# Kernel tuning notes

Measured on AMD Instinct MI355X. Metric: run time of the kernel, lower is better.

Reference implementation:

```python
import jax, jax.numpy as jnp
import numpy as np

EPS = 1e-10


def _cotangent(V, F):
    # V: (B,N,3) float, F: (B,Fc,3) int -> C: (B,Fc,3) cotangent weights for edges 23,31,12
    gather = jax.vmap(lambda v, f: v[f])  # (N,3),(Fc,3) -> (Fc,3,3)
    vi = gather(V, F)
    v1, v2, v3 = vi[:, :, 0, :], vi[:, :, 1, :], vi[:, :, 2, :]
    l1 = jnp.sqrt(((v2 - v3) ** 2).sum(-1))
    l2 = jnp.sqrt(((v3 - v1) ** 2).sum(-1))
    l3 = jnp.sqrt(((v1 - v2) ** 2).sum(-1))
    sp = (l1 + l2 + l3) * 0.5
    inside = sp * (sp - l1) * (sp - l2) * (sp - l3)
    inside = jnp.maximum(inside, 0.0)
    A = 2.0 * jnp.sqrt(inside)
    cot23 = l2 ** 2 + l3 ** 2 - l1 ** 2
    cot31 = l1 ** 2 + l3 ** 2 - l2 ** 2
    cot12 = l1 ** 2 + l2 ** 2 - l3 ** 2
    C = jnp.stack([cot23, cot31, cot12], axis=2) / (A[:, :, None] + EPS) / 4.0
    C = jnp.where(A[:, :, None] == 0.0, 0.0, C)
    return C


def setup_inputs() -> dict:
    key = jax.random.key(0)
    k1, k2 = jax.random.split(key)
    B, N, Fc = 8, 100000, 200000
    V = jax.random.normal(k1, (B, N, 3), dtype=jnp.float32)
    F = jax.random.randint(k2, (B, Fc, 3), 0, N, dtype=jnp.int64)
    return {"V": V, "F": F}


def reference(V, F):
    B, N, _ = V.shape
    BN = B * N
    # Laplacian weights are built once from V and treated as constants
    # (the original torch autograd.Function never differentiates through L).
    C = _cotangent(jax.lax.stop_gradient(V), F)  # (B,Fc,3)
    offset = (jnp.arange(B, dtype=F.dtype) * N)[:, None, None]
    Fb = (F + offset).reshape(-1, 3)             # (B*Fc,3) global vertex ids
    rows = Fb[:, jnp.array([1, 2, 0])].reshape(-1)
    cols = Fb[:, jnp.array([2, 0, 1])].reshape(-1)
    w = C.reshape(-1)                             # matches rows/cols ordering

    Vf = V.reshape(BN, 3)
    # Lx where L = A + A^T - diag(rowsum(A + A^T)), A = sparse(rows,cols,w)
    out = jnp.zeros((BN, 3), dtype=V.dtype)
    out = out.at[rows].add(w[:, None] * Vf[cols])
    out = out.at[cols].add(w[:, None] * Vf[rows])
    deg = jnp.zeros((BN,), dtype=V.dtype)
    deg = deg.at[rows].add(w).at[cols].add(w)
    out = out - deg[:, None] * Vf
    return out.reshape(B, N, 3)
```

## Files before the change

### kernel.cpp

```cpp
#include <hip/hip_runtime.h>

#define NBATCH 8
#define NSEG   4

#define RANGE_BIG  13312
#define RANGE_SM   5120

struct I3 { int a, b, c; };
struct P3 { float x, y, z; };

__device__ __forceinline__ void cot_weights(
    const P3& p0, const P3& p1, const P3& p2,
    float& w0, float& w1, float& w2)
{
    const float EPSf = 1e-10f;
    float dx, dy, dz;
    dx = p1.x - p2.x; dy = p1.y - p2.y; dz = p1.z - p2.z;
    float l1 = sqrtf(dx * dx + dy * dy + dz * dz);
    dx = p2.x - p0.x; dy = p2.y - p0.y; dz = p2.z - p0.z;
    float l2 = sqrtf(dx * dx + dy * dy + dz * dz);
    dx = p0.x - p1.x; dy = p0.y - p1.y; dz = p0.z - p1.z;
    float l3 = sqrtf(dx * dx + dy * dy + dz * dz);

    float sp = (l1 + l2 + l3) * 0.5f;
    float inside = sp * (sp - l1) * (sp - l2) * (sp - l3);
    inside = fmaxf(inside, 0.0f);
    float A = 2.0f * sqrtf(inside);
    float denom = A + EPSf;

    float l1s = l1 * l1, l2s = l2 * l2, l3s = l3 * l3;
    w0 = (l2s + l3s - l1s) / denom * 0.25f;
    w1 = (l1s + l3s - l2s) / denom * 0.25f;
    w2 = (l1s + l2s - l3s) / denom * 0.25f;
    if (A == 0.0f) { w0 = 0.0f; w1 = 0.0f; w2 = 0.0f; }
}

__device__ __forceinline__ void gather_body(
    const float* __restrict__ V, const int* __restrict__ F,
    float* __restrict__ part, float* lacc,
    int N, int Fc, int BN3, int range, int nr, int nthreads)
{
    int b  = blockIdx.x % NBATCH;
    int t  = blockIdx.x / NBATCH;
    int r  = t / NSEG;
    int s  = t % NSEG;
    if (r >= nr) return;

    int lo = r * range;
    int hi = min(lo + range, N);
    unsigned rlen = (unsigned)(hi - lo);
    int len3 = (hi - lo) * 3;

    for (int i = threadIdx.x; i < len3; i += nthreads) lacc[i] = 0.0f;
    __syncthreads();

    int fps = (Fc + NSEG - 1) / NSEG;
    int f0 = s * fps;
    int f1 = min(f0 + fps, Fc);

    const int*   Fb = F + (size_t)b * Fc * 3;
    const float* Vb = V + (size_t)b * N * 3;

    for (int f = f0 + (int)threadIdx.x; f < f1; f += nthreads) {
        I3 idx = *reinterpret_cast<const I3*>(Fb + (size_t)f * 3);
        unsigned u0 = (unsigned)(idx.a - lo);
        unsigned u1 = (unsigned)(idx.b - lo);
        unsigned u2 = (unsigned)(idx.c - lo);
        bool in0 = u0 < rlen, in1 = u1 < rlen, in2 = u2 < rlen;
        if (!(in0 || in1 || in2)) continue;

        P3 p0 = *reinterpret_cast<const P3*>(Vb + (size_t)idx.a * 3);
        P3 p1 = *reinterpret_cast<const P3*>(Vb + (size_t)idx.b * 3);
        P3 p2 = *reinterpret_cast<const P3*>(Vb + (size_t)idx.c * 3);

        float w0, w1, w2;
        cot_weights(p0, p1, p2, w0, w1, w2);

        if (in0) {
            atomicAdd(&lacc[u0 * 3 + 0], w1 * (p2.x - p0.x) + w2 * (p1.x - p0.x));
            atomicAdd(&lacc[u0 * 3 + 1], w1 * (p2.y - p0.y) + w2 * (p1.y - p0.y));
            atomicAdd(&lacc[u0 * 3 + 2], w1 * (p2.z - p0.z) + w2 * (p1.z - p0.z));
        }
        if (in1) {
            atomicAdd(&lacc[u1 * 3 + 0], w0 * (p2.x - p1.x) + w2 * (p0.x - p1.x));
            atomicAdd(&lacc[u1 * 3 + 1], w0 * (p2.y - p1.y) + w2 * (p0.y - p1.y));
            atomicAdd(&lacc[u1 * 3 + 2], w0 * (p2.z - p1.z) + w2 * (p0.z - p1.z));
        }
        if (in2) {
            atomicAdd(&lacc[u2 * 3 + 0], w0 * (p1.x - p2.x) + w1 * (p0.x - p2.x));
            atomicAdd(&lacc[u2 * 3 + 1], w0 * (p1.y - p2.y) + w1 * (p0.y - p2.y));
            atomicAdd(&lacc[u2 * 3 + 2], w0 * (p1.z - p2.z) + w1 * (p0.z - p2.z));
        }
    }
    __syncthreads();

    float* dst = part + (size_t)s * BN3 + ((size_t)b * N + lo) * 3;
    for (int i = threadIdx.x; i < len3; i += nthreads) dst[i] = lacc[i];
}

__global__ void __launch_bounds__(1024, 1) cot_gather_big(
    const float* __restrict__ V, const int* __restrict__ F,
    float* __restrict__ part, int N, int Fc, int BN3)
{
    extern __shared__ float lacc_dyn[];
    int nr = (N + RANGE_BIG - 1) / RANGE_BIG;
    gather_body(V, F, part, lacc_dyn, N, Fc, BN3, RANGE_BIG, nr, 1024);
}

__global__ void __launch_bounds__(512) cot_gather_sm(
    const float* __restrict__ V, const int* __restrict__ F,
    float* __restrict__ part, int N, int Fc, int BN3)
{
    __shared__ float lacc_st[RANGE_SM * 3];
    int nr = (N + RANGE_SM - 1) / RANGE_SM;
    gather_body(V, F, part, lacc_st, N, Fc, BN3, RANGE_SM, nr, 512);
}

__global__ void __launch_bounds__(256) cot_merge4(
    const float* __restrict__ part, float* __restrict__ out, int BN3)
{
    int i = blockIdx.x * blockDim.x + threadIdx.x;
    int n4 = BN3 >> 2;
    if (i >= n4) return;
    float4 a = ((const float4*)part)[i];
#pragma unroll
    for (int s = 1; s < NSEG; ++s) {
        float4 p = ((const float4*)(part + (size_t)s * BN3))[i];
        a.x += p.x; a.y += p.y; a.z += p.z; a.w += p.w;
    }
    ((float4*)out)[i] = a;
}

__global__ void __launch_bounds__(256) cot_merge1(
    const float* __restrict__ part, float* __restrict__ out, int BN3)
{
    int i = blockIdx.x * blockDim.x + threadIdx.x;
    if (i >= BN3) return;
    float v = part[i];
#pragma unroll
    for (int s = 1; s < NSEG; ++s) v += part[(size_t)s * BN3 + i];
    out[i] = v;
}

__global__ void __launch_bounds__(256) cot_face_add9(
    const float* __restrict__ V, const int* __restrict__ F,
    float* __restrict__ out, int N, int Fc)
{
    int idx = blockIdx.x * blockDim.x + threadIdx.x;
    int total = NBATCH * Fc;
    if (idx >= total) return;

    int b = idx / Fc;
    I3 ix = *reinterpret_cast<const I3*>(F + (size_t)idx * 3);
    int vb = b * N;
    int g0 = vb + ix.a, g1 = vb + ix.b, g2 = vb + ix.c;

    P3 p0 = *reinterpret_cast<const P3*>(V + (size_t)g0 * 3);
    P3 p1 = *reinterpret_cast<const P3*>(V + (size_t)g1 * 3);
    P3 p2 = *reinterpret_cast<const P3*>(V + (size_t)g2 * 3);

    float w0, w1, w2;
    cot_weights(p0, p1, p2, w0, w1, w2);

    atomicAdd(&out[(size_t)g0 * 3 + 0], w1 * (p2.x - p0.x) + w2 * (p1.x - p0.x));
    atomicAdd(&out[(size_t)g0 * 3 + 1], w1 * (p2.y - p0.y) + w2 * (p1.y - p0.y));
    atomicAdd(&out[(size_t)g0 * 3 + 2], w1 * (p2.z - p0.z) + w2 * (p1.z - p0.z));
    atomicAdd(&out[(size_t)g1 * 3 + 0], w0 * (p2.x - p1.x) + w2 * (p0.x - p1.x));
    atomicAdd(&out[(size_t)g1 * 3 + 1], w0 * (p2.y - p1.y) + w2 * (p0.y - p1.y));
    atomicAdd(&out[(size_t)g1 * 3 + 2], w0 * (p2.z - p1.z) + w2 * (p0.z - p1.z));
    atomicAdd(&out[(size_t)g2 * 3 + 0], w0 * (p1.x - p2.x) + w1 * (p0.x - p2.x));
    atomicAdd(&out[(size_t)g2 * 3 + 1], w0 * (p1.y - p2.y) + w1 * (p0.y - p2.y));
    atomicAdd(&out[(size_t)g2 * 3 + 2], w0 * (p1.z - p2.z) + w1 * (p0.z - p2.z));
}

extern "C" void kernel_launch(void* const* d_in, const int* in_sizes, int n_in,
                              void* d_out, int out_size, void* d_ws, size_t ws_size,
                              hipStream_t stream) {
    const float* V = (const float*)d_in[0];
    const int*   F = (const int*)d_in[1];
    float* out = (float*)d_out;

    int BN3 = in_sizes[0];
    int N   = BN3 / (NBATCH * 3);
    int Fc  = in_sizes[1] / (NBATCH * 3);

    size_t need = (size_t)NSEG * BN3 * sizeof(float);

    if (ws_size >= need) {
        const int dynLds = RANGE_BIG * 3 * sizeof(float);
        hipError_t attr_ok = hipFuncSetAttribute(
            reinterpret_cast<const void*>(cot_gather_big),
            hipFuncAttributeMaxDynamicSharedMemorySize, dynLds);

        if (attr_ok == hipSuccess) {
            int nr = (N + RANGE_BIG - 1) / RANGE_BIG;
            int gblocks = NBATCH * nr * NSEG;
            cot_gather_big<<<gblocks, 1024, dynLds, stream>>>(V, F, (float*)d_ws, N, Fc, BN3);
        } else {
            int nr = (N + RANGE_SM - 1) / RANGE_SM;
            int gblocks = NBATCH * nr * NSEG;
            cot_gather_sm<<<gblocks, 512, 0, stream>>>(V, F, (float*)d_ws, N, Fc, BN3);
        }

        if ((BN3 & 3) == 0) {
            int mblocks = ((BN3 >> 2) + 255) / 256;
            cot_merge4<<<mblocks, 256, 0, stream>>>((const float*)d_ws, out, BN3);
        } else {
            int mblocks = (BN3 + 255) / 256;
            cot_merge1<<<mblocks, 256, 0, stream>>>((const float*)d_ws, out, BN3);
        }
    } else {
        hipMemsetAsync(d_out, 0, (size_t)BN3 * sizeof(float), stream);
        int totalF = NBATCH * Fc;
        int fblocks = (totalF + 255) / 256;
        cot_face_add9<<<fblocks, 256, 0, stream>>>(V, F, out, N, Fc);
    }
}
```

Measured before the change: 168.2 us.

## Precompute per-face cotangent contributions once before range-partitioned LDS scatter

New measurement: 201.2 us. 19.6% more time.

```diff
diff --git a/kernel.cpp b/kernel.cpp
--- a/kernel.cpp
+++ b/kernel.cpp
@@ -1,10 +1,8 @@
 #include <hip/hip_runtime.h>
 
 #define NBATCH 8
-#define NSEG   4
-
 #define RANGE_BIG  13312
-#define RANGE_SM   5120
+#define MAXSEG 4
 
 struct I3 { int a, b, c; };
 struct P3 { float x, y, z; };
@@ -35,43 +33,158 @@
     if (A == 0.0f) { w0 = 0.0f; w1 = 0.0f; w2 = 0.0f; }
 }
 
-__device__ __forceinline__ void gather_body(
+__global__ void __launch_bounds__(256) cot_prep(
     const float* __restrict__ V, const int* __restrict__ F,
-    float* __restrict__ part, float* lacc,
-    int N, int Fc, int BN3, int range, int nr, int nthreads)
-{
-    int b  = blockIdx.x % NBATCH;
-    int t  = blockIdx.x / NBATCH;
-    int r  = t / NSEG;
-    int s  = t % NSEG;
+    float* __restrict__ cbuf, int N, int Fc)
+{
+    int idx = blockIdx.x * blockDim.x + threadIdx.x;
+    int total = NBATCH * Fc;
+    if (idx >= total) return;
+
+    int b = idx / Fc;
+    I3 ix = *reinterpret_cast<const I3*>(F + (size_t)idx * 3);
+    const float* Vb = V + (size_t)b * N * 3;
+    P3 p0 = *reinterpret_cast<const P3*>(Vb + (size_t)ix.a * 3);
+    P3 p1 = *reinterpret_cast<const P3*>(Vb + (size_t)ix.b * 3);
+    P3 p2 = *reinterpret_cast<const P3*>(Vb + (size_t)ix.c * 3);
+
+    float w0, w1, w2;
+    cot_weights(p0, p1, p2, w0, w1, w2);
+
+    float* c = cbuf + (size_t)idx * 9;
+    c[0] = w1 * (p2.x - p0.x) + w2 * (p1.x - p0.x);
+    c[1] = w1 * (p2.y - p0.y) + w2 * (p1.y - p0.y);
+    c[2] = w1 * (p2.z - p0.z) + w2 * (p1.z - p0.z);
+    c[3] = w0 * (p2.x - p1.x) + w2 * (p0.x - p1.x);
+    c[4] = w0 * (p2.y - p1.y) + w2 * (p0.y - p1.y);
+    c[5] = w0 * (p2.z - p1.z) + w2 * (p0.z - p1.z);
+    c[6] = w0 * (p1.x - p2.x) + w1 * (p0.x - p2.x);
+    c[7] = w0 * (p1.y - p2.y) + w1 * (p0.y - p2.y);
+    c[8] = w0 * (p1.z - p2.z) + w1 * (p0.z - p2.z);
+}
+
+__global__ void __launch_bounds__(1024, 1) cot_scatter_big(
+    const int*   __restrict__ F, const float* __restrict__ cbuf,
+    float*       __restrict__ part, int N, int Fc, int BN3, int nseg)
+{
+    extern __shared__ float lacc[];
+    int nr = (N + RANGE_BIG - 1) / RANGE_BIG;
+
+    int b = blockIdx.x % NBATCH;
+    int t = blockIdx.x / NBATCH;
+    int r = t / nseg;
+    int s = t % nseg;
     if (r >= nr) return;
 
-    int lo = r * range;
-    int hi = min(lo + range, N);
+    int lo = r * RANGE_BIG;
+    int hi = min(lo + RANGE_BIG, N);
     unsigned rlen = (unsigned)(hi - lo);
     int len3 = (hi - lo) * 3;
 
-    for (int i = threadIdx.x; i < len3; i += nthreads) lacc[i] = 0.0f;
+    for (int i = threadIdx.x; i < len3; i += 1024) lacc[i] = 0.0f;
     __syncthreads();
 
-    int fps = (Fc + NSEG - 1) / NSEG;
+    int fps = (Fc + nseg - 1) / nseg;
     int f0 = s * fps;
     int f1 = min(f0 + fps, Fc);
 
     const int*   Fb = F + (size_t)b * Fc * 3;
-    const float* Vb = V + (size_t)b * N * 3;
-
-    for (int f = f0 + (int)threadIdx.x; f < f1; f += nthreads) {
-        I3 idx = *reinterpret_cast<const I3*>(Fb + (size_t)f * 3);
-        unsigned u0 = (unsigned)(idx.a - lo);
-        unsigned u1 = (unsigned)(idx.b - lo);
-        unsigned u2 = (unsigned)(idx.c - lo);
+    const float* Cb = cbuf + (size_t)b * Fc * 9;
+
+    for (int f = f0 + (int)threadIdx.x; f < f1; f += 1024) {
+        I3 ix = *reinterpret_cast<const I3*>(Fb + (size_t)f * 3);
+        unsigned u0 = (unsigned)(ix.a - lo);
+        unsigned u1 = (unsigned)(ix.b - lo);
+        unsigned u2 = (unsigned)(ix.c - lo);
         bool in0 = u0 < rlen, in1 = u1 < rlen, in2 = u2 < rlen;
         if (!(in0 || in1 || in2)) continue;
 
-        P3 p0 = *reinterpret_cast<const P3*>(Vb + (size_t)idx.a * 3);
-        P3 p1 = *reinterpret_cast<const P3*>(Vb + (size_t)idx.b * 3);
-        P3 p2 = *reinterpret_cast<const P3*>(Vb + (size_t)idx.c * 3);
+        const float* c = Cb + (size_t)f * 9;
+        if (in0) {
+            atomicAdd(&lacc[u0 * 3 + 0], c[0]);
+            atomicAdd(&lacc[u0 * 3 + 1], c[1]);
+            atomicAdd(&lacc[u0 * 3 + 2], c[2]);
+        }
+        if (in1) {
+            atomicAdd(&lacc[u1 * 3 + 0], c[3]);
+            atomicAdd(&lacc[u1 * 3 + 1], c[4]);
+            atomicAdd(&lacc[u1 * 3 + 2], c[5]);
+        }
+        if (in2) {
+            atomicAdd(&lacc[u2 * 3 + 0], c[6]);
+            atomicAdd(&lacc[u2 * 3 + 1], c[7]);
+            atomicAdd(&lacc[u2 * 3 + 2], c[8]);
+        }
+    }
+    __syncthreads();
+
+    float* dst = part + (size_t)s * BN3 + ((size_t)b * N + lo) * 3;
+    for (int i = threadIdx.x; i < len3; i += 1024) dst[i] = lacc[i];
+}
+
+__global__ void __launch_bounds__(256) cot_merge4(
+    const float* __restrict__ part, float* __restrict__ out, int BN3, int nseg)
+{
+    int i = blockIdx.x * blockDim.x + threadIdx.x;
+    int n4 = BN3 >> 2;
+    if (i >= n4) return;
+    float4 a = ((const float4*)part)[i];
+    for (int s = 1; s < nseg; ++s) {
+        float4 p = ((const float4*)(part + (size_t)s * BN3))[i];
+        a.x += p.x; a.y += p.y; a.z += p.z; a.w += p.w;
+    }
+    ((float4*)out)[i] = a;
+}
+
+__global__ void __launch_bounds__(256) cot_merge1(
+    const float* __restrict__ part, float* __restrict__ out, int BN3, int nseg)
+{
+    int i = blockIdx.x * blockDim.x + threadIdx.x;
+    if (i >= BN3) return;
+    float v = part[i];
+    for (int s = 1; s < nseg; ++s) v += part[(size_t)s * BN3 + i];
+    out[i] = v;
+}
+
+__global__ void __launch_bounds__(1024, 1) cot_gather_big(
+    const float* __restrict__ V, const int* __restrict__ F,
+    float* __restrict__ part, int N, int Fc, int BN3, int nseg)
+{
+    extern __shared__ float lacc[];
+    int nr = (N + RANGE_BIG - 1) / RANGE_BIG;
+
+    int b = blockIdx.x % NBATCH;
+    int t = blockIdx.x / NBATCH;
+    int r = t / nseg;
+    int s = t % nseg;
+    if (r >= nr) return;
+
+    int lo = r * RANGE_BIG;
+    int hi = min(lo + RANGE_BIG, N);
+    unsigned rlen = (unsigned)(hi - lo);
+    int len3 = (hi - lo) * 3;
+
+    for (int i = threadIdx.x; i < len3; i += 1024) lacc[i] = 0.0f;
+    __syncthreads();
+
+    int fps = (Fc + nseg - 1) / nseg;
+    int f0 = s * fps;
+    int f1 = min(f0 + fps, Fc);
+
+    const int*   Fb = F + (size_t)b * Fc * 3;
+    const float* Vb = V + (size_t)b * N * 3;
+
+    for (int f = f0 + (int)threadIdx.x; f < f1; f += 1024) {
+        I3 ix = *reinterpret_cast<const I3*>(Fb + (size_t)f * 3);
+        unsigned u0 = (unsigned)(ix.a - lo);
+        unsigned u1 = (unsigned)(ix.b - lo);
+        unsigned u2 = (unsigned)(ix.c - lo);
+        bool in0 = u0 < rlen, in1 = u1 < rlen, in2 = u2 < rlen;
+        if (!(in0 || in1 || in2)) continue;
+
+        P3 p0 = *reinterpret_cast<const P3*>(Vb + (size_t)ix.a * 3);
+        P3 p1 = *reinterpret_cast<const P3*>(Vb + (size_t)ix.b * 3);
+        P3 p2 = *reinterpret_cast<const P3*>(Vb + (size_t)ix.c * 3);
 
         float w0, w1, w2;
         cot_weights(p0, p1, p2, w0, w1, w2);
@@ -95,51 +208,7 @@
     __syncthreads();
 
     float* dst = part + (size_t)s * BN3 + ((size_t)b * N + lo) * 3;
-    for (int i = threadIdx.x; i < len3; i += nthreads) dst[i] = lacc[i];
-}
-
-__global__ void __launch_bounds__(1024, 1) cot_gather_big(
-    const float* __restrict__ V, const int* __restrict__ F,
-    float* __restrict__ part, int N, int Fc, int BN3)
-{
-    extern __shared__ float lacc_dyn[];
-    int nr = (N + RANGE_BIG - 1) / RANGE_BIG;
-    gather_body(V, F, part, lacc_dyn, N, Fc, BN3, RANGE_BIG, nr, 1024);
-}
-
-__global__ void __launch_bounds__(512) cot_gather_sm(
-    const float* __restrict__ V, const int* __restrict__ F,
-    float* __restrict__ part, int N, int Fc, int BN3)
-{
-    __shared__ float lacc_st[RANGE_SM * 3];
-    int nr = (N + RANGE_SM - 1) / RANGE_SM;
-    gather_body(V, F, part, lacc_st, N, Fc, BN3, RANGE_SM, nr, 512);
-}
-
-__global__ void __launch_bounds__(256) cot_merge4(
-    const float* __restrict__ part, float* __restrict__ out, int BN3)
-{
-    int i = blockIdx.x * blockDim.x + threadIdx.x;
-    int n4 = BN3 >> 2;
-    if (i >= n4) return;
-    float4 a = ((const float4*)part)[i];
-#pragma unroll
-    for (int s = 1; s < NSEG; ++s) {
-        float4 p = ((const float4*)(part + (size_t)s * BN3))[i];
-        a.x += p.x; a.y += p.y; a.z += p.z; a.w += p.w;
-    }
-    ((float4*)out)[i] = a;
-}
-
-__global__ void __launch_bounds__(256) cot_merge1(
-    const float* __restrict__ part, float* __restrict__ out, int BN3)
-{
-    int i = blockIdx.x * blockDim.x + threadIdx.x;
-    if (i >= BN3) return;
-    float v = part[i];
-#pragma unroll
-    for (int s = 1; s < NSEG; ++s) v += part[(size_t)s * BN3 + i];
-    out[i] = v;
+    for (int i = threadIdx.x; i < len3; i += 1024) dst[i] = lacc[i];
 }
 
 __global__ void __launch_bounds__(256) cot_face_add9(
@@ -183,36 +252,61 @@
     int BN3 = in_sizes[0];
     int N   = BN3 / (NBATCH * 3);
     int Fc  = in_sizes[1] / (NBATCH * 3);
-
-    size_t need = (size_t)NSEG * BN3 * sizeof(float);
-
-    if (ws_size >= need) {
-        const int dynLds = RANGE_BIG * 3 * sizeof(float);
-        hipError_t attr_ok = hipFuncSetAttribute(
-            reinterpret_cast<const void*>(cot_gather_big),
+    int totalF = NBATCH * Fc;
+
+    size_t cbytes = (size_t)totalF * 9 * sizeof(float);
+    size_t pbytes = (size_t)BN3 * sizeof(float);
+
+    int nseg = 0;
+    for (int s = MAXSEG; s >= 1; --s)
+        if (ws_size >= cbytes + (size_t)s * pbytes) { nseg = s; break; }
+
+    const int dynLds = RANGE_BIG * 3 * sizeof(float);
+    int nr = (N + RANGE_BIG - 1) / RANGE_BIG;
+
+    if (nseg > 0) {
+        hipError_t ok = hipFuncSetAttribute(
+            reinterpret_cast<const void*>(cot_scatter_big),
             hipFuncAttributeMaxDynamicSharedMemorySize, dynLds);
-
-        if (attr_ok == hipSuccess) {
-            int nr = (N + RANGE_BIG - 1) / RANGE_BIG;
-            int gblocks = NBATCH * nr * NSEG;
-            cot_gather_big<<<gblocks, 1024, dynLds, stream>>>(V, F, (float*)d_ws, N, Fc, BN3);
-        } else {
-            int nr = (N + RANGE_SM - 1) / RANGE_SM;
-            int gblocks = NBATCH * nr * NSEG;
-            cot_gather_sm<<<gblocks, 512, 0, stream>>>(V, F, (float*)d_ws, N, Fc, BN3);
-        }
-
+        if (ok == hipSuccess) {
+            float* cbuf = (float*)d_ws;
+            float* part = (float*)((char*)d_ws + cbytes);
+
+            int pblocks = (totalF + 255) / 256;
+            cot_prep<<<pblocks, 256, 0, stream>>>(V, F, cbuf, N, Fc);
+
+            int sblocks = NBATCH * nr * nseg;
+            cot_scatter_big<<<sblocks, 1024, dynLds, stream>>>(F, cbuf, part, N, Fc, BN3, nseg);
+
+            if ((BN3 & 3) == 0) {
+                int mblocks = ((BN3 >> 2) + 255) / 256;
+                cot_merge4<<<mblocks, 256, 0, stream>>>(part, out, BN3, nseg);
+            } else {
+                int mblocks = (BN3 + 255) / 256;
+                cot_merge1<<<mblocks, 256, 0, stream>>>(part, out, BN3, nseg);
+            }
+            return;
+        }
+    }
+
+    if (ws_size >= 4 * pbytes &&
+        hipFuncSetAttribute(reinterpret_cast<const void*>(cot_gather_big),
+                            hipFuncAttributeMaxDynamicSharedMemorySize,
+                            dynLds) == hipSuccess) {
+        int fseg = 4;
+        int gblocks = NBATCH * nr * fseg;
+        cot_gather_big<<<gblocks, 1024, dynLds, stream>>>(V, F, (float*)d_ws, N, Fc, BN3, fseg);
         if ((BN3 & 3) == 0) {
             int mblocks = ((BN3 >> 2) + 255) / 256;
-            cot_merge4<<<mblocks, 256, 0, stream>>>((const float*)d_ws, out, BN3);
+            cot_merge4<<<mblocks, 256, 0, stream>>>((const float*)d_ws, out, BN3, fseg);
         } else {
             int mblocks = (BN3 + 255) / 256;
-            cot_merge1<<<mblocks, 256, 0, stream>>>((const float*)d_ws, out, BN3);
-        }
-    } else {
-        hipMemsetAsync(d_out, 0, (size_t)BN3 * sizeof(float), stream);
-        int totalF = NBATCH * Fc;
-        int fblocks = (totalF + 255) / 256;
-        cot_face_add9<<<fblocks, 256, 0, stream>>>(V, F, out, N, Fc);
-    }
-}
+            cot_merge1<<<mblocks, 256, 0, stream>>>((const float*)d_ws, out, BN3, fseg);
+        }
+        return;
+    }
+
+    hipMemsetAsync(d_out, 0, (size_t)BN3 * sizeof(float), stream);
+    int fblocks = (totalF + 255) / 256;
+    cot_face_add9<<<fblocks, 256, 0, stream>>>(V, F, out, N, Fc);
+}
```
